# Kernel tuning notes

Measured on AMD Instinct MI355X. Metric: run time of the kernel, lower is better.

Reference implementation:

```python
import jax, jax.numpy as jnp
import numpy as np

B, L, E, H, D = 4, 4096, 1024, 16, 64  # batch, seq, embed, heads, head_dim
EPS = 1e-6


def setup_inputs() -> dict:
    key = jax.random.key(0)
    k1, k2, k3 = jax.random.split(key, 3)
    return {
        "q": jax.random.normal(k1, (B, L, E), dtype=jnp.float32),
        "k": jax.random.normal(k2, (B, L, E), dtype=jnp.float32),
        "v": jax.random.normal(k3, (B, L, E), dtype=jnp.float32),
        "mask": jnp.ones((B, L), dtype=jnp.float32),
    }


def _split_heads(x):
    # (B, L, E) -> (B*H, L, D)
    return x.reshape(B, L, H, D).transpose(0, 2, 1, 3).reshape(B * H, L, D)


def reference(q, k, v, mask):
    # feature map: relu
    q = jax.nn.relu(q)
    k = jax.nn.relu(k)
    # padding mask applied to keys/values
    k = k * mask[:, :, None]
    v = v * mask[:, :, None]
    q = _split_heads(q)
    k = _split_heads(k)
    v = _split_heads(v)
    # cosFormer sin/cos reweighting: pi/2 * i / m for i = 1..L
    idx = (np.pi / 2) * jnp.arange(1, L + 1, dtype=jnp.float32) / L
    s = jnp.sin(idx)[None, :, None]  # (1, L, 1)
    c = jnp.cos(idx)[None, :, None]
    q_ = jnp.concatenate([q * s, q * c], axis=-1)  # (B*H, L, 2D)
    k_ = jnp.concatenate([k * s, k * c], axis=-1)
    # linear-attention KV accumulation (non-causal): (B*H, 2D, D)
    kv = jnp.einsum('nld,nlm->ndm', k_, v)
    # normalizer
    z = 1.0 / jnp.maximum(jnp.einsum('nld,nd->nl', q_, k_.sum(axis=1)), EPS)
    out = jnp.einsum('nld,ndm,nl->nlm', q_, kv, z)  # (B*H, L, D)
    return out.reshape(B, H, L, D)
```

## Files before the change

### kernel.cpp

```cpp
#include <hip/hip_runtime.h>
#include <hip/hip_bf16.h>
#include <math.h>

#define B_ 4
#define L_ 4096
#define E_ 1024
#define H_ 16
#define D_ 64
#define N_ 64
#define D2_ 128
#define EPS_ 1e-6f

#define CH_ 8
#define LC_ (L_ / CH_)
#define LT_ 64
#define NST_ (LC_ / LT_)

#define DANG_ 3.83495197e-4f

typedef short short8 __attribute__((ext_vector_type(8)));
typedef float f32x4 __attribute__((ext_vector_type(4)));
typedef unsigned int u32;
typedef unsigned short u16;

static __device__ __forceinline__ u32 pack2bf(float a, float b) {
  union { __hip_bfloat16 h; u16 s; } x, y;
  x.h = __float2bfloat16(a);
  y.h = __float2bfloat16(b);
  return (u32)x.s | ((u32)y.s << 16);
}

static __device__ __forceinline__ short bf1(float a) {
  union { __hip_bfloat16 h; short s; } x;
  x.h = __float2bfloat16(a);
  return x.s;
}

static __device__ __forceinline__ void gld16(const void* g, void* l) {
  __builtin_amdgcn_global_load_lds(
      (const __attribute__((address_space(1))) unsigned int*)g,
      (__attribute__((address_space(3))) unsigned int*)l, 16, 0, 0);
}

__global__ __launch_bounds__(256, 3) void phase1_mfma(
    const float* __restrict__ k, const float* __restrict__ v,
    const float* __restrict__ mask,
    float* __restrict__ part_kv, float* __restrict__ part_ks) {
  __shared__ __align__(16) u16 ka[D2_ * 72];
  __shared__ __align__(16) u16 vt[D_ * 72];

  const int bid = blockIdx.x;
  const int n = bid & 63;
  const int ch = bid >> 6;
  const int b = n >> 4;
  const int h = n & 15;
  const int t = threadIdx.x;
  const int wv = t >> 6;
  const int lane = t & 63;
  const int c_lo = lane & 15;
  const int lp = lane >> 4;
  const int c = wv * 16 + c_lo;

  f32x4 acc[2][4];
#pragma unroll
  for (int i = 0; i < 2; ++i)
#pragma unroll
    for (int j = 0; j < 4; ++j) acc[i][j] = (f32x4)0.f;
  float kss = 0.f, ksc = 0.f;

  const int l0 = ch * LC_;
  const size_t gb0 = (size_t)(b * L_ + l0) * E_ + h * 64 + c;

  float Ak0[8], Ak1[8], Av0[8], Av1[8], Am;
  float Bk0[8], Bk1[8], Bv0[8], Bv1[8], Bm;

#define P1_PREF(Rk0, Rk1, Rv0, Rv1, Rm, S)                                   \
  do {                                                                       \
    const size_t gs_ = gb0 + (size_t)(S) * (LT_ * E_);                       \
    _Pragma("unroll") for (int i_ = 0; i_ < 8; ++i_) {                       \
      const size_t g0_ = gs_ + (size_t)(8 * i_ + 2 * lp) * E_;               \
      Rk0[i_] = k[g0_];                                                      \
      Rk1[i_] = k[g0_ + E_];                                                 \
      Rv0[i_] = v[g0_];                                                      \
      Rv1[i_] = v[g0_ + E_];                                                 \
    }                                                                        \
    Rm = mask[(size_t)b * L_ + l0 + (S) * LT_ + lane];                       \
  } while (0)

#define P1_STAGE(Rk0, Rk1, Rv0, Rv1, Rm, S)                                  \
  do {                                                                       \
    const int lb_ = l0 + (S) * LT_;                                          \
    _Pragma("unroll") for (int i_ = 0; i_ < 8; ++i_) {                       \
      const int l_ = 8 * i_ + 2 * lp;                                        \
      const float m0_ = __shfl(Rm, l_);                                      \
      const float m1_ = __shfl(Rm, l_ + 1);                                  \
      float s0_, c0_, s1_, c1_;                                              \
      __sincosf((float)(lb_ + l_ + 1) * DANG_, &s0_, &c0_);                  \
      __sincosf((float)(lb_ + l_ + 2) * DANG_, &s1_, &c1_);                  \
      const float kr0_ = fmaxf(Rk0[i_], 0.f) * m0_;                          \
      const float kr1_ = fmaxf(Rk1[i_], 0.f) * m1_;                          \
      const float ks0_ = kr0_ * s0_, ks1_ = kr1_ * s1_;                      \
      const float kc0_ = kr0_ * c0_, kc1_ = kr1_ * c1_;                      \
      const int li_ = 4 * i_ + lp;                                           \
      ((u32*)ka)[c * 36 + li_] = pack2bf(ks0_, ks1_);                        \
      ((u32*)ka)[(c + 64) * 36 + li_] = pack2bf(kc0_, kc1_);                 \
      ((u32*)vt)[c * 36 + li_] = pack2bf(Rv0[i_] * m0_, Rv1[i_] * m1_);      \
      kss += ks0_ + ks1_;                                                    \
      ksc += kc0_ + kc1_;                                                    \
    }                                                                        \
  } while (0)

#define P1_MMA()                                                             \
  do {                                                                       \
    _Pragma("unroll") for (int kk_ = 0; kk_ < 2; ++kk_) {                    \
      const int colo_ = kk_ * 32 + lp * 8;                                   \
      short8 af_[2], bf_[4];                                                 \
      _Pragma("unroll") for (int dt_ = 0; dt_ < 2; ++dt_)                    \
          af_[dt_] =                                                         \
              *(const short8*)&ka[(wv * 32 + dt_ * 16 + c_lo) * 72 + colo_]; \
      _Pragma("unroll") for (int mt_ = 0; mt_ < 4; ++mt_)                    \
          bf_[mt_] = *(const short8*)&vt[(mt_ * 16 + c_lo) * 72 + colo_];    \
      _Pragma("unroll") for (int dt_ = 0; dt_ < 2; ++dt_)                    \
          _Pragma("unroll") for (int mt_ = 0; mt_ < 4; ++mt_)                \
              acc[dt_][mt_] = __builtin_amdgcn_mfma_f32_16x16x32_bf16(       \
                  af_[dt_], bf_[mt_], acc[dt_][mt_], 0, 0, 0);               \
    }                                                                        \
  } while (0)

  P1_PREF(Ak0, Ak1, Av0, Av1, Am, 0);
  for (int st = 0; st < NST_; st += 2) {
    __syncthreads();
    P1_PREF(Bk0, Bk1, Bv0, Bv1, Bm, st + 1);
    P1_STAGE(Ak0, Ak1, Av0, Av1, Am, st);
    __syncthreads();
    P1_MMA();
    __syncthreads();
    if (st + 2 < NST_) P1_PREF(Ak0, Ak1, Av0, Av1, Am, st + 2);
    P1_STAGE(Bk0, Bk1, Bv0, Bv1, Bm, st + 1);
    __syncthreads();
    P1_MMA();
  }

  const size_t pbase = (size_t)(ch * N_ + n) * (D2_ * D_);
#pragma unroll
  for (int dt = 0; dt < 2; ++dt) {
    const int d = wv * 32 + dt * 16 + lp * 4;
#pragma unroll
    for (int mt = 0; mt < 4; ++mt) {
      const int mcol = mt * 16 + c_lo;
#pragma unroll
      for (int r = 0; r < 4; ++r)
        part_kv[pbase + (size_t)(d + r) * D_ + mcol] = acc[dt][mt][r];
    }
  }
  kss += __shfl_xor(kss, 16); kss += __shfl_xor(kss, 32);
  ksc += __shfl_xor(ksc, 16); ksc += __shfl_xor(ksc, 32);
  if (lp == 0) {
    part_ks[(size_t)(ch * N_ + n) * D2_ + c] = kss;
    part_ks[(size_t)(ch * N_ + n) * D2_ + c + 64] = ksc;
  }
}

__global__ __launch_bounds__(256) void reduce_t(
    const float* __restrict__ part_kv, const float* __restrict__ part_ks,
    u16* __restrict__ kvt, float* __restrict__ ks) {
  __shared__ __align__(16) float tsh[16 * 68];
  const int bid = blockIdx.x;
  const int n = bid >> 3;
  const int sl = bid & 7;
  const int t = threadIdx.x;

  const int e0 = sl * 1024 + t * 4;
  f32x4 s = (f32x4)0.f;
#pragma unroll
  for (int cc = 0; cc < CH_; ++cc)
    s += *(const f32x4*)&part_kv[(size_t)(cc * N_ + n) * (D2_ * D_) + e0];
  *(f32x4*)&tsh[(t >> 4) * 68 + (t & 15) * 4] = s;

  if (sl == 0 && t < D2_) {
    float ss = 0.f;
#pragma unroll
    for (int cc = 0; cc < CH_; ++cc)
      ss += part_ks[(size_t)(cc * N_ + n) * D2_ + t];
    ks[n * D2_ + t] = ss;
  }
  __syncthreads();

  const int m = t >> 2;
  const int d4 = (t & 3) * 4;
  const u32 lo = pack2bf(tsh[(d4 + 0) * 68 + m], tsh[(d4 + 1) * 68 + m]);
  const u32 hi = pack2bf(tsh[(d4 + 2) * 68 + m], tsh[(d4 + 3) * 68 + m]);
  uint2 pk; pk.x = lo; pk.y = hi;
  *(uint2*)&kvt[(size_t)n * (D2_ * D_) + (size_t)m * D2_ + sl * 16 + d4] = pk;
}

__global__ __launch_bounds__(256, 4) void phase2_mfma(
    const float* __restrict__ q, const u16* __restrict__ kvt,
    const float* __restrict__ ks, float* __restrict__ out) {
  __shared__ __align__(16) float qsh[64 * 64];
  __shared__ __align__(16) u16 kbsh[64 * 128];

  const int bid = blockIdx.x;
  const int n = bid & 63;
  const int lc = bid >> 6;
  const int b = n >> 4, h = n & 15;
  const int t = threadIdx.x;
  const int wv = t >> 6, lane = t & 63;
  const int c_lo = lane & 15, quad = lane >> 4;
  const int l0 = lc * 64;

  const float* qbase = q + (size_t)(b * L_ + l0) * E_ + h * 64;
  const u16* kvbase = kvt + (size_t)n * (D2_ * D_);
  const int rsub = lane >> 4;
  const int g = lane & 15;
#pragma unroll
  for (int j = 0; j < 4; ++j) {
    const int r = wv * 16 + j * 4 + rsub;
    gld16(qbase + (size_t)r * E_ + ((g ^ (r & 15)) << 2),
          qsh + (wv * 16 + j * 4) * 64);
    gld16(kvbase + (size_t)r * D2_ + ((g ^ (r & 15)) << 3),
          kbsh + (wv * 16 + j * 4) * 128);
  }

  const float* ksn = ks + n * D2_;
  short8 bks[4];
#pragma unroll
  for (int kk = 0; kk < 4; ++kk) {
    const f32x4 ka_ = *(const f32x4*)(ksn + kk * 32 + quad * 8);
    const f32x4 kb_ = *(const f32x4*)(ksn + kk * 32 + quad * 8 + 4);
    short8 tt = {0, 0, 0, 0, 0, 0, 0, 0};
    if (c_lo == 0) {
#pragma unroll
      for (int j = 0; j < 4; ++j) {
        tt[j] = bf1(ka_[j]);
        tt[j + 4] = bf1(kb_[j]);
      }
    }
    bks[kk] = tt;
  }

  const int row = wv * 16 + c_lo;
  float sv, cv;
  __sincosf((float)(l0 + row + 1) * DANG_, &sv, &cv);

  __syncthreads();

  const float* qrow = qsh + row * 64;
  const int sw = row & 15;
  const f32x4 a0 = *(const f32x4*)(qrow + (((2 * quad) ^ sw) << 2));
  const f32x4 a1 = *(const f32x4*)(qrow + (((2 * quad + 1) ^ sw) << 2));
  const f32x4 a2 = *(const f32x4*)(qrow + (((8 + 2 * quad) ^ sw) << 2));
  const f32x4 a3 = *(const f32x4*)(qrow + (((9 + 2 * quad) ^ sw) << 2));

  short8 af[4];
#pragma unroll
  for (int j = 0; j < 4; ++j) {
    const float x0 = fmaxf(a0[j], 0.f);
    const float x1 = fmaxf(a1[j], 0.f);
    const float x2 = fmaxf(a2[j], 0.f);
    const float x3 = fmaxf(a3[j], 0.f);
    af[0][j] = bf1(x0 * sv); af[0][j + 4] = bf1(x1 * sv);
    af[1][j] = bf1(x2 * sv); af[1][j + 4] = bf1(x3 * sv);
    af[2][j] = bf1(x0 * cv); af[2][j + 4] = bf1(x1 * cv);
    af[3][j] = bf1(x2 * cv); af[3][j + 4] = bf1(x3 * cv);
  }

  f32x4 acc[4];
#pragma unroll
  for (int mt = 0; mt < 4; ++mt) acc[mt] = (f32x4)0.f;
  f32x4 acc5 = (f32x4)0.f;

#pragma unroll
  for (int kk = 0; kk < 4; ++kk) {
#pragma unroll
    for (int mt = 0; mt < 4; ++mt) {
      const int m = mt * 16 + c_lo;
      const short8 bfr = *(const short8*)
          &kbsh[m * 128 + (((kk * 4 + quad) ^ (m & 15)) << 3)];
      acc[mt] = __builtin_amdgcn_mfma_f32_16x16x32_bf16(af[kk], bfr, acc[mt], 0, 0, 0);
    }
    acc5 = __builtin_amdgcn_mfma_f32_16x16x32_bf16(af[kk], bks[kk], acc5, 0, 0, 0);
  }

#pragma unroll
  for (int r = 0; r < 4; ++r) {
    const float den = __shfl(acc5[r], quad * 16);
    const float z = 1.f / fmaxf(den, EPS_);
    const int gl = l0 + wv * 16 + quad * 4 + r;
    const size_t ob = (size_t)n * (L_ * D_) + (size_t)gl * D_;
#pragma unroll
    for (int mt = 0; mt < 4; ++mt)
      out[ob + mt * 16 + c_lo] = acc[mt][r] * z;
  }
}

extern "C" void kernel_launch(void* const* d_in, const int* in_sizes, int n_in,
                              void* d_out, int out_size, void* d_ws,
                              size_t ws_size, hipStream_t stream) {
  const float* q = (const float*)d_in[0];
  const float* k = (const float*)d_in[1];
  const float* v = (const float*)d_in[2];
  const float* mask = (const float*)d_in[3];
  float* out = (float*)d_out;

  float* part_kv = (float*)d_ws;
  float* part_ks = part_kv + (size_t)CH_ * N_ * D2_ * D_;
  u16* kvt = (u16*)(part_ks + (size_t)CH_ * N_ * D2_);
  float* ks = (float*)(kvt + (size_t)N_ * D2_ * D_);

  phase1_mfma<<<dim3(CH_ * N_), dim3(256), 0, stream>>>(k, v, mask, part_kv, part_ks);
  reduce_t<<<dim3(N_ * 8), dim3(256), 0, stream>>>(part_kv, part_ks, kvt, ks);
  phase2_mfma<<<dim3(N_ * 64), dim3(256), 0, stream>>>(q, kvt, ks, out);
}
```

Measured before the change: 296.9 us.

## Double-buffer phase1 LDS, split L into more chunks, process two row tiles per phase2 block

```diff
diff --git a/kernel.cpp b/kernel.cpp
--- a/kernel.cpp
+++ b/kernel.cpp
@@ -11,7 +11,7 @@
 #define D2_ 128
 #define EPS_ 1e-6f
 
-#define CH_ 8
+#define CH_ 16
 #define LC_ (L_ / CH_)
 #define LT_ 64
 #define NST_ (LC_ / LT_)
@@ -42,12 +42,12 @@
       (__attribute__((address_space(3))) unsigned int*)l, 16, 0, 0);
 }
 
-__global__ __launch_bounds__(256, 3) void phase1_mfma(
+__global__ __launch_bounds__(256, 2) void phase1_mfma(
     const float* __restrict__ k, const float* __restrict__ v,
     const float* __restrict__ mask,
     float* __restrict__ part_kv, float* __restrict__ part_ks) {
-  __shared__ __align__(16) u16 ka[D2_ * 72];
-  __shared__ __align__(16) u16 vt[D_ * 72];
+  __shared__ __align__(16) u16 ka[2][D2_ * 72];
+  __shared__ __align__(16) u16 vt[2][D_ * 72];
 
   const int bid = blockIdx.x;
   const int n = bid & 63;
@@ -87,7 +87,7 @@
     Rm = mask[(size_t)b * L_ + l0 + (S) * LT_ + lane];                       \
   } while (0)
 
-#define P1_STAGE(Rk0, Rk1, Rv0, Rv1, Rm, S)                                  \
+#define P1_STAGE(Rk0, Rk1, Rv0, Rv1, Rm, S, BUF)                             \
   do {                                                                       \
     const int lb_ = l0 + (S) * LT_;                                          \
     _Pragma("unroll") for (int i_ = 0; i_ < 8; ++i_) {                       \
@@ -102,24 +102,25 @@
       const float ks0_ = kr0_ * s0_, ks1_ = kr1_ * s1_;                      \
       const float kc0_ = kr0_ * c0_, kc1_ = kr1_ * c1_;                      \
       const int li_ = 4 * i_ + lp;                                           \
-      ((u32*)ka)[c * 36 + li_] = pack2bf(ks0_, ks1_);                        \
-      ((u32*)ka)[(c + 64) * 36 + li_] = pack2bf(kc0_, kc1_);                 \
-      ((u32*)vt)[c * 36 + li_] = pack2bf(Rv0[i_] * m0_, Rv1[i_] * m1_);      \
+      ((u32*)ka[BUF])[c * 36 + li_] = pack2bf(ks0_, ks1_);                   \
+      ((u32*)ka[BUF])[(c + 64) * 36 + li_] = pack2bf(kc0_, kc1_);            \
+      ((u32*)vt[BUF])[c * 36 + li_] = pack2bf(Rv0[i_] * m0_, Rv1[i_] * m1_); \
       kss += ks0_ + ks1_;                                                    \
       ksc += kc0_ + kc1_;                                                    \
     }                                                                        \
   } while (0)
 
-#define P1_MMA()                                                             \
+#define P1_MMA(BUF)                                                          \
   do {                                                                       \
     _Pragma("unroll") for (int kk_ = 0; kk_ < 2; ++kk_) {                    \
       const int colo_ = kk_ * 32 + lp * 8;                                   \
       short8 af_[2], bf_[4];                                                 \
       _Pragma("unroll") for (int dt_ = 0; dt_ < 2; ++dt_)                    \
-          af_[dt_] =                                                         \
-              *(const short8*)&ka[(wv * 32 + dt_ * 16 + c_lo) * 72 + colo_]; \
+          af_[dt_] = *(const short8*)                                        \
+              &ka[BUF][(wv * 32 + dt_ * 16 + c_lo) * 72 + colo_];            \
       _Pragma("unroll") for (int mt_ = 0; mt_ < 4; ++mt_)                    \
-          bf_[mt_] = *(const short8*)&vt[(mt_ * 16 + c_lo) * 72 + colo_];    \
+          bf_[mt_] = *(const short8*)                                        \
+              &vt[BUF][(mt_ * 16 + c_lo) * 72 + colo_];                      \
       _Pragma("unroll") for (int dt_ = 0; dt_ < 2; ++dt_)                    \
           _Pragma("unroll") for (int mt_ = 0; mt_ < 4; ++mt_)                \
               acc[dt_][mt_] = __builtin_amdgcn_mfma_f32_16x16x32_bf16(       \
@@ -128,17 +129,27 @@
   } while (0)
 
   P1_PREF(Ak0, Ak1, Av0, Av1, Am, 0);
+  P1_STAGE(Ak0, Ak1, Av0, Av1, Am, 0, 0);
+  if (2 < NST_) P1_PREF(Ak0, Ak1, Av0, Av1, Am, 2);
+  P1_PREF(Bk0, Bk1, Bv0, Bv1, Bm, 1);
+  __syncthreads();
+
+#pragma unroll
   for (int st = 0; st < NST_; st += 2) {
+    if (st + 1 < NST_) {
+      P1_STAGE(Bk0, Bk1, Bv0, Bv1, Bm, st + 1, 1);
+      if (st + 3 < NST_) P1_PREF(Bk0, Bk1, Bv0, Bv1, Bm, st + 3);
+    }
+    P1_MMA(0);
     __syncthreads();
-    P1_PREF(Bk0, Bk1, Bv0, Bv1, Bm, st + 1);
-    P1_STAGE(Ak0, Ak1, Av0, Av1, Am, st);
-    __syncthreads();
-    P1_MMA();
-    __syncthreads();
-    if (st + 2 < NST_) P1_PREF(Ak0, Ak1, Av0, Av1, Am, st + 2);
-    P1_STAGE(Bk0, Bk1, Bv0, Bv1, Bm, st + 1);
-    __syncthreads();
-    P1_MMA();
+    if (st + 1 < NST_) {
+      if (st + 2 < NST_) {
+        P1_STAGE(Ak0, Ak1, Av0, Av1, Am, st + 2, 0);
+        if (st + 4 < NST_) P1_PREF(Ak0, Ak1, Av0, Av1, Am, st + 4);
+      }
+      P1_MMA(1);
+      __syncthreads();
+    }
   }
 
   const size_t pbase = (size_t)(ch * N_ + n) * (D2_ * D_);
@@ -194,20 +205,20 @@
   *(uint2*)&kvt[(size_t)n * (D2_ * D_) + (size_t)m * D2_ + sl * 16 + d4] = pk;
 }
 
-__global__ __launch_bounds__(256, 4) void phase2_mfma(
+__global__ __launch_bounds__(256, 3) void phase2_mfma(
     const float* __restrict__ q, const u16* __restrict__ kvt,
     const float* __restrict__ ks, float* __restrict__ out) {
-  __shared__ __align__(16) float qsh[64 * 64];
+  __shared__ __align__(16) float qsh[2 * 64 * 64];
   __shared__ __align__(16) u16 kbsh[64 * 128];
 
   const int bid = blockIdx.x;
   const int n = bid & 63;
-  const int lc = bid >> 6;
+  const int g2 = bid >> 6;
   const int b = n >> 4, h = n & 15;
   const int t = threadIdx.x;
   const int wv = t >> 6, lane = t & 63;
   const int c_lo = lane & 15, quad = lane >> 4;
-  const int l0 = lc * 64;
+  const int l0 = g2 * 128;
 
   const float* qbase = q + (size_t)(b * L_ + l0) * E_ + h * 64;
   const u16* kvbase = kvt + (size_t)n * (D2_ * D_);
@@ -216,10 +227,13 @@
 #pragma unroll
   for (int j = 0; j < 4; ++j) {
     const int r = wv * 16 + j * 4 + rsub;
-    gld16(qbase + (size_t)r * E_ + ((g ^ (r & 15)) << 2),
+    const int sw = (g ^ (r & 15));
+    gld16(kvbase + (size_t)r * D2_ + (sw << 3),
+          kbsh + (wv * 16 + j * 4) * 128);
+    gld16(qbase + (size_t)r * E_ + (sw << 2),
           qsh + (wv * 16 + j * 4) * 64);
-    gld16(kvbase + (size_t)r * D2_ + ((g ^ (r & 15)) << 3),
-          kbsh + (wv * 16 + j * 4) * 128);
+    gld16(qbase + (size_t)(64 + r) * E_ + (sw << 2),
+          qsh + 4096 + (wv * 16 + j * 4) * 64);
   }
 
   const float* ksn = ks + n * D2_;
@@ -239,58 +253,63 @@
     bks[kk] = tt;
   }
 
-  const int row = wv * 16 + c_lo;
-  float sv, cv;
-  __sincosf((float)(l0 + row + 1) * DANG_, &sv, &cv);
-
   __syncthreads();
 
-  const float* qrow = qsh + row * 64;
-  const int sw = row & 15;
-  const f32x4 a0 = *(const f32x4*)(qrow + (((2 * quad) ^ sw) << 2));
-  const f32x4 a1 = *(const f32x4*)(qrow + (((2 * quad + 1) ^ sw) << 2));
-  const f32x4 a2 = *(const f32x4*)(qrow + (((8 + 2 * quad) ^ sw) << 2));
-  const f32x4 a3 = *(const f32x4*)(qrow + (((9 + 2 * quad) ^ sw) << 2));
-
-  short8 af[4];
-#pragma unroll
-  for (int j = 0; j < 4; ++j) {
-    const float x0 = fmaxf(a0[j], 0.f);
-    const float x1 = fmaxf(a1[j], 0.f);
-    const float x2 = fmaxf(a2[j], 0.f);
-    const float x3 = fmaxf(a3[j], 0.f);
-    af[0][j] = bf1(x0 * sv); af[0][j + 4] = bf1(x1 * sv);
-    af[1][j] = bf1(x2 * sv); af[1][j + 4] = bf1(x3 * sv);
-    af[2][j] = bf1(x0 * cv); af[2][j + 4] = bf1(x1 * cv);
-    af[3][j] = bf1(x2 * cv); af[3][j + 4] = bf1(x3 * cv);
-  }
-
-  f32x4 acc[4];
-#pragma unroll
-  for (int mt = 0; mt < 4; ++mt) acc[mt] = (f32x4)0.f;
-  f32x4 acc5 = (f32x4)0.f;
-
-#pragma unroll
-  for (int kk = 0; kk < 4; ++kk) {
-#pragma unroll
-    for (int mt = 0; mt < 4; ++mt) {
-      const int m = mt * 16 + c_lo;
-      const short8 bfr = *(const short8*)
-          &kbsh[m * 128 + (((kk * 4 + quad) ^ (m & 15)) << 3)];
-      acc[mt] = __builtin_amdgcn_mfma_f32_16x16x32_bf16(af[kk], bfr, acc[mt], 0, 0, 0);
-    }
-    acc5 = __builtin_amdgcn_mfma_f32_16x16x32_bf16(af[kk], bks[kk], acc5, 0, 0, 0);
-  }
-
-#pragma unroll
-  for (int r = 0; r < 4; ++r) {
-    const float den = __shfl(acc5[r], quad * 16);
-    const float z = 1.f / fmaxf(den, EPS_);
-    const int gl = l0 + wv * 16 + quad * 4 + r;
-    const size_t ob = (size_t)n * (L_ * D_) + (size_t)gl * D_;
-#pragma unroll
-    for (int mt = 0; mt < 4; ++mt)
-      out[ob + mt * 16 + c_lo] = acc[mt][r] * z;
+#pragma unroll
+  for (int cc = 0; cc < 2; ++cc) {
+    const int row = wv * 16 + c_lo;
+    const int glr = l0 + cc * 64 + row;
+    float sv, cv;
+    __sincosf((float)(glr + 1) * DANG_, &sv, &cv);
+
+    const float* qrow = qsh + cc * 4096 + row * 64;
+    const int sw = row & 15;
+    const f32x4 a0 = *(const f32x4*)(qrow + (((2 * quad) ^ sw) << 2));
+    const f32x4 a1 = *(const f32x4*)(qrow + (((2 * quad + 1) ^ sw) << 2));
+    const f32x4 a2 = *(const f32x4*)(qrow + (((8 + 2 * quad) ^ sw) << 2));
+    const f32x4 a3 = *(const f32x4*)(qrow + (((9 + 2 * quad) ^ sw) << 2));
+
+    short8 af[4];
+#pragma unroll
+    for (int j = 0; j < 4; ++j) {
+      const float x0 = fmaxf(a0[j], 0.f);
+      const float x1 = fmaxf(a1[j], 0.f);
+      const float x2 = fmaxf(a2[j], 0.f);
+      const float x3 = fmaxf(a3[j], 0.f);
+      af[0][j] = bf1(x0 * sv); af[0][j + 4] = bf1(x1 * sv);
+      af[1][j] = bf1(x2 * sv); af[1][j + 4] = bf1(x3 * sv);
+      af[2][j] = bf1(x0 * cv); af[2][j + 4] = bf1(x1 * cv);
+      af[3][j] = bf1(x2 * cv); af[3][j + 4] = bf1(x3 * cv);
+    }
+
+    f32x4 acc[4];
+#pragma unroll
+    for (int mt = 0; mt < 4; ++mt) acc[mt] = (f32x4)0.f;
+    f32x4 acc5 = (f32x4)0.f;
+
+#pragma unroll
+    for (int kk = 0; kk < 4; ++kk) {
+#pragma unroll
+      for (int mt = 0; mt < 4; ++mt) {
+        const int m = mt * 16 + c_lo;
+        const short8 bfr = *(const short8*)
+            &kbsh[m * 128 + (((kk * 4 + quad) ^ (m & 15)) << 3)];
+        acc[mt] =
+            __builtin_amdgcn_mfma_f32_16x16x32_bf16(af[kk], bfr, acc[mt], 0, 0, 0);
+      }
+      acc5 = __builtin_amdgcn_mfma_f32_16x16x32_bf16(af[kk], bks[kk], acc5, 0, 0, 0);
+    }
+
+#pragma unroll
+    for (int r = 0; r < 4; ++r) {
+      const float den = __shfl(acc5[r], quad * 16);
+      const float z = 1.f / fmaxf(den, EPS_);
+      const int gl = l0 + cc * 64 + wv * 16 + quad * 4 + r;
+      const size_t ob = (size_t)n * (L_ * D_) + (size_t)gl * D_;
+#pragma unroll
+      for (int mt = 0; mt < 4; ++mt)
+        out[ob + mt * 16 + c_lo] = acc[mt][r] * z;
+    }
   }
 }
 
@@ -310,5 +329,5 @@
 
   phase1_mfma<<<dim3(CH_ * N_), dim3(256), 0, stream>>>(k, v, mask, part_kv, part_ks);
   reduce_t<<<dim3(N_ * 8), dim3(256), 0, stream>>>(part_kv, part_ks, kvt, ks);
-  phase2_mfma<<<dim3(N_ * 64), dim3(256), 0, stream>>>(q, kvt, ks, out);
-}
+  phase2_mfma<<<dim3(N_ * 32), dim3(256), 0, stream>>>(q, kvt, ks, out);
+}
```

Result: faster. 251.5 us (-15.3%).
